# Kernel tuning notes

Hardware: AMD Instinct MI355X
Metric: run time of the kernel (lower is better)

Reference implementation:

```python
import jax, jax.numpy as jnp
import numpy as np

OUTLINER_RATIO = 0.01
RANK = 16
SVD_NITER = 2  # matches torch.svd_lowrank default


def _randomized_svd(A, rank, key, niter=SVD_NITER):
    # torch.svd_lowrank-style randomized range finder + small SVD.
    n, d = A.shape
    Omega = jax.random.normal(key, (d, rank), dtype=A.dtype)
    Q, _ = jnp.linalg.qr(A @ Omega)               # [n, rank]
    for _ in range(niter):
        Q, _ = jnp.linalg.qr(A.T @ Q)             # [d, rank]
        Q, _ = jnp.linalg.qr(A @ Q)               # [n, rank]
    B = Q.T @ A                                   # [rank, d]
    Ub, S, Vh = jnp.linalg.svd(B, full_matrices=False)
    U = Q @ Ub                                    # [n, rank]
    return U, S, Vh


def get_statistics(x, outliner_ratio):
    # threshold such that ~outliner_ratio fraction of |x| exceeds it
    return jnp.quantile(jnp.abs(x), 1.0 - outliner_ratio)


def compress(x, outliner, rank, key):
    # split outliers (kept exactly) from sub-outlier part (low-rank compressed)
    x_outlier = jnp.where(jnp.abs(x) > outliner, x, jnp.zeros((), x.dtype))
    x_sub = (x - x_outlier).reshape(-1, x.shape[-1])   # [N, D]
    U, S, Vh = _randomized_svd(x_sub, rank, key)
    R = Vh.T                                           # [D, rank]
    Rinv = Vh                                          # orthonormal -> pinv = transpose
    L = x_sub @ R                                      # [N, rank]
    return x_outlier, L, R, Rinv


def reference(x, iteration):
    result = jax.nn.silu(x)
    # iteration < 10 branch: compute fresh outlier statistics
    outliner = get_statistics(x, OUTLINER_RATIO)
    # iteration % 50 == 0 -> execute_svd = True (iteration = 0 here)
    key = jax.random.key(42)
    x_outlier_compressed, L, R, Rinv = compress(x, outliner, RANK, key)
    return result, outliner, R, Rinv


def setup_inputs() -> dict:
    key = jax.random.key(0)
    x = jax.random.normal(key, (4, 2048, 4096), dtype=jnp.float32)
    return {"x": x, "iteration": 0}
```

## Files before the change

kernel.cpp:

```cpp
#include <hip/hip_runtime.h>
#include <math.h>


#define N_TOTAL 33554432
#define DDIM    4096
#define NROWS   8192
#define NCHUNK  32
#define RTARGET 33218888u

__device__ __forceinline__ double frcp(double x){
  double r = (double)(1.0f/(float)x);
  r = r*(2.0 - x*r);
  r = r*(2.0 - x*r);
  return r;
}
__device__ __forceinline__ double frsqrt(double x){
  double r = (double)rsqrtf((float)x);
  double hx = 0.5*x;
  r = r*(1.5 - hx*r*r);
  r = r*(1.5 - hx*r*r);
  return r;
}
__device__ __forceinline__ double fsqrt(double x){
  return (x == 0.0) ? 0.0 : x*frsqrt(x);
}

__device__ __forceinline__ double dsign(double a, double b){ return (b >= 0.0) ? fabs(a) : -fabs(a); }

__device__ __forceinline__ void f_slartg(double f, double g, double& c, double& s, double& r){
  if (g == 0.0){ c=1.0; s=0.0; r=f; }
  else if (f == 0.0){ c=0.0; s=dsign(1.0,g); r=fabs(g); }
  else {
    double d2 = f*f+g*g;
    double inv = frsqrt(d2);
    c = fabs(f)*inv;
    r = dsign(d2*inv, f);
    s = g*inv*dsign(1.0,f);
  }
}

__device__ void f_slas2(double f, double g, double h, double& ssmin, double& ssmax){
  double fa=fabs(f), ga=fabs(g), ha=fabs(h);
  double fhmn=fmin(fa,ha), fhmx=fmax(fa,ha);
  if (fhmn == 0.0){
    ssmin=0.0;
    if (fhmx==0.0) ssmax=ga;
    else { double mx=fmax(fhmx,ga), mn=fmin(fhmx,ga); double q=mn*frcp(mx); ssmax = mx*fsqrt(1.0+q*q); }
  } else {
    if (ga < fhmx){
      double rinv = frcp(fhmx);
      double as_=1.0+fhmn*rinv, at=(fhmx-fhmn)*rinv, au=ga*rinv; au=au*au;
      double c=2.0*frcp(fsqrt(as_*as_+au)+fsqrt(at*at+au));
      ssmin=fhmn*c; ssmax=fhmx*frcp(c);
    } else {
      double au=fhmx*frcp(ga);
      if (au==0.0){ ssmin=(fhmn*fhmx)*frcp(ga); ssmax=ga; }
      else {
        double rinv = frcp(fhmx);
        double as_=1.0+fhmn*rinv, at=(fhmx-fhmn)*rinv;
        double c=frcp(fsqrt(1.0+(as_*au)*(as_*au))+fsqrt(1.0+(at*au)*(at*au)));
        ssmin=(fhmn*c)*au; ssmin=ssmin+ssmin; ssmax=ga*frcp(c+c);
      }
    }
  }
}

__device__ void f_slasv2(double f, double g, double h,
                         double& ssmin, double& ssmax, double& snr, double& csr, double& snl, double& csl){
  const double EPSd = 5.9604645e-8;
  double ft=f, fa=fabs(f), ht=h, ha=fabs(h);
  int pmax=1;
  bool swap_=(ha>fa);
  if (swap_){ pmax=3; double t=ft; ft=ht; ht=t; t=fa; fa=ha; ha=t; }
  double gt=g, ga=fabs(g);
  double clt=0, crt=0, slt=0, srt=0;
  if (ga == 0.0){ ssmin=ha; ssmax=fa; clt=1; crt=1; slt=0; srt=0; }
  else {
    bool gasmal=true;
    if (ga > fa){
      pmax=2;
      if ((fa*frcp(ga)) < EPSd){
        gasmal=false;
        ssmax=ga;
        ssmin = (ha>1.0) ? (fa*frcp(ga*frcp(ha))) : ((fa*frcp(ga))*ha);
        clt=1; slt=ht*frcp(gt); srt=1; crt=ft*frcp(gt);
      }
    }
    if (gasmal){
      double d_=fa-ha;
      double fainv = frcp(fa);
      double l_=(d_==fa)?1.0:(d_*fainv);
      double m_=gt*frcp(ft);
      double t_=2.0-l_;
      double mm=m_*m_, tt=t_*t_;
      double s_=fsqrt(tt+mm);
      double r_=(l_==0.0)?fabs(m_):fsqrt(l_*l_+mm);
      double a_=0.5*(s_+r_);
      double ainv = frcp(a_);
      ssmin=ha*ainv;
      ssmax=fa*a_;
      if (mm==0.0){
        t_=(l_==0.0)?(dsign(2.0,ft)*dsign(1.0,gt)):(gt*frcp(dsign(d_,ft))+m_*frcp(t_));
      } else {
        t_=(m_*frcp(s_+t_)+m_*frcp(r_+l_))*(1.0+a_);
      }
      l_=fsqrt(t_*t_+4.0);
      double linv = frcp(l_);
      crt=2.0*linv;
      srt=t_*linv;
      clt=(crt+srt*m_)*ainv;
      slt=(ht*frcp(ft))*srt*ainv;
    }
  }
  if (swap_){ csl=srt; snl=crt; csr=slt; snr=clt; }
  else { csl=clt; snl=slt; csr=crt; snr=srt; }
  double tsign=0.0;
  if (pmax==1) tsign = dsign(1.0,csr)*dsign(1.0,csl)*dsign(1.0,f);
  if (pmax==2) tsign = dsign(1.0,snr)*dsign(1.0,csl)*dsign(1.0,g);
  if (pmax==3) tsign = dsign(1.0,snr)*dsign(1.0,snl)*dsign(1.0,h);
  ssmax = dsign(ssmax, tsign);
  ssmin = dsign(ssmin, tsign*dsign(1.0,f)*dsign(1.0,h));
}

__global__ __launch_bounds__(256) void k_hist1(const float4* __restrict__ x4, unsigned* __restrict__ h1){
  __shared__ unsigned lh[4096];
  for (int i=threadIdx.x; i<4096; i+=256) lh[i]=0u;
  __syncthreads();
  int tid = blockIdx.x*blockDim.x + threadIdx.x;
  int stride = gridDim.x*blockDim.x;
  for (int i = tid; i < N_TOTAL/4; i += stride){
    float4 v = x4[i];
    atomicAdd(&lh[(__float_as_uint(v.x)&0x7FFFFFFFu)>>19], 1u);
    atomicAdd(&lh[(__float_as_uint(v.y)&0x7FFFFFFFu)>>19], 1u);
    atomicAdd(&lh[(__float_as_uint(v.z)&0x7FFFFFFFu)>>19], 1u);
    atomicAdd(&lh[(__float_as_uint(v.w)&0x7FFFFFFFu)>>19], 1u);
  }
  __syncthreads();
  for (int i=threadIdx.x; i<4096; i+=256){ unsigned c=lh[i]; if (c) atomicAdd(&h1[i], c); }
}

__global__ __launch_bounds__(256) void k_siluhist(const float4* __restrict__ x4, float4* __restrict__ o4,
                                                  unsigned* __restrict__ h1){
  __shared__ unsigned lh[4096];
  for (int i=threadIdx.x; i<4096; i+=256) lh[i]=0u;
  __syncthreads();
  int tid = blockIdx.x*blockDim.x + threadIdx.x;
  int stride = gridDim.x*blockDim.x;
  for (int i = tid; i < N_TOTAL/4; i += stride){
    float4 v = x4[i];
    float4 o;
    o.x = v.x / (1.0f + expf(-v.x));
    o.y = v.y / (1.0f + expf(-v.y));
    o.z = v.z / (1.0f + expf(-v.z));
    o.w = v.w / (1.0f + expf(-v.w));
    o4[i] = o;
    atomicAdd(&lh[(__float_as_uint(v.x)&0x7FFFFFFFu)>>19], 1u);
    atomicAdd(&lh[(__float_as_uint(v.y)&0x7FFFFFFFu)>>19], 1u);
    atomicAdd(&lh[(__float_as_uint(v.z)&0x7FFFFFFFu)>>19], 1u);
    atomicAdd(&lh[(__float_as_uint(v.w)&0x7FFFFFFFu)>>19], 1u);
  }
  __syncthreads();
  for (int i=threadIdx.x; i<4096; i+=256){ unsigned c=lh[i]; if (c) atomicAdd(&h1[i], c); }
}

__global__ __launch_bounds__(1024) void k_select1(const unsigned* __restrict__ h1, unsigned* __restrict__ sel){
  __shared__ unsigned ssum[1024];
  int t = threadIdx.x;
  unsigned psum = 0;
  for (int k=0;k<4;++k) psum += h1[t*4+k];
  ssum[t]=psum; __syncthreads();
  for (int off=1; off<1024; off<<=1){
    unsigned v = (t>=off)? ssum[t-off]:0u;
    __syncthreads();
    ssum[t] += v;
    __syncthreads();
  }
  unsigned incl = ssum[t], excl = incl - psum;
  if (excl <= RTARGET && RTARGET < incl){
    unsigned run = excl;
    for (int k=0;k<4;++k){
      unsigned c = h1[t*4+k];
      if (run + c > RTARGET){ sel[1]=(unsigned)(t*4+k); sel[2]=RTARGET-run; break; }
      run += c;
    }
  }
}

__global__ void k_hist2(const float4* __restrict__ x4, unsigned* __restrict__ h2, const unsigned* __restrict__ sel){
  unsigned hstar = sel[1];
  int tid = blockIdx.x*blockDim.x + threadIdx.x;
  int stride = gridDim.x*blockDim.x;
  for (int i = tid; i < N_TOTAL/4; i += stride){
    float4 v = x4[i];
    unsigned b;
    b = __float_as_uint(v.x) & 0x7FFFFFFFu; if ((b>>19)==hstar) atomicAdd(&h2[b&0x7FFFFu],1u);
    b = __float_as_uint(v.y) & 0x7FFFFFFFu; if ((b>>19)==hstar) atomicAdd(&h2[b&0x7FFFFu],1u);
    b = __float_as_uint(v.z) & 0x7FFFFFFFu; if ((b>>19)==hstar) atomicAdd(&h2[b&0x7FFFFu],1u);
    b = __float_as_uint(v.w) & 0x7FFFFFFFu; if ((b>>19)==hstar) atomicAdd(&h2[b&0x7FFFFu],1u);
  }
}

__global__ __launch_bounds__(128) void k_grpsum(const uint4* __restrict__ h2v, unsigned* __restrict__ gs){
  __shared__ unsigned red[128];
  int g = blockIdx.x, t = threadIdx.x;
  uint4 v = h2v[(size_t)g*128 + t];
  red[t] = v.x+v.y+v.z+v.w;
  __syncthreads();
  for (int off=64; off; off>>=1){ if (t<off) red[t] += red[t+off]; __syncthreads(); }
  if (t==0) gs[g] = red[0];
}

__global__ __launch_bounds__(1024) void k_select2b(const unsigned* __restrict__ gs, const unsigned* __restrict__ h2,
                                                   unsigned* __restrict__ sel, float* __restrict__ outScalar){
  __shared__ unsigned ssum[1024];
  __shared__ unsigned sg[2];
  int t = threadIdx.x;
  unsigned target = sel[2], hstar = sel[1];
  unsigned psum = gs[t];
  ssum[t]=psum; __syncthreads();
  for (int off=1; off<1024; off<<=1){
    unsigned v = (t>=off)? ssum[t-off]:0u;
    __syncthreads();
    ssum[t] += v;
    __syncthreads();
  }
  unsigned incl = ssum[t], excl = incl - psum;
  if (excl <= target && target < incl){ sg[0]=(unsigned)t; sg[1]=excl; }
  __syncthreads();
  unsigned g = sg[0], gexcl = sg[1];
  unsigned cnt = (t<512) ? h2[(size_t)g*512 + t] : 0u;
  __syncthreads();
  ssum[t]=cnt; __syncthreads();
  for (int off=1; off<1024; off<<=1){
    unsigned v = (t>=off)? ssum[t-off]:0u;
    __syncthreads();
    ssum[t] += v;
    __syncthreads();
  }
  unsigned incl2 = ssum[t], excl2 = incl2 - cnt;
  unsigned rem = target - gexcl;
  if (t < 512 && excl2 <= rem && rem < incl2){
    unsigned tb = (hstar<<19) | (g*512 + (unsigned)t);
    float tv = __uint_as_float(tb);
    ((float*)sel)[0] = tv;
    *outScalar = tv;
  }
}

__device__ __forceinline__ unsigned rotl32(unsigned x, int r){ return (x<<r)|(x>>(32-r)); }

__device__ __forceinline__ float bits_to_normal(unsigned g){
  float u01 = __uint_as_float((g>>9) | 0x3F800000u) - 1.0f;
  float u = __fadd_rn(__fmul_rn(u01, 2.0f), -0.99999994f);
  u = fmaxf(-0.99999994f, u);
  float xx = __fmul_rn(u,u);
  float w = -log1pf(-xx);
  float p;
  if (w < 5.0f){
    w = __fadd_rn(w, -2.5f);
    p = 2.81022636e-08f;
    p = __fadd_rn(3.43273939e-07f, __fmul_rn(p,w));
    p = __fadd_rn(-3.5233877e-06f, __fmul_rn(p,w));
    p = __fadd_rn(-4.39150654e-06f, __fmul_rn(p,w));
    p = __fadd_rn(0.00021858087f, __fmul_rn(p,w));
    p = __fadd_rn(-0.00125372503f, __fmul_rn(p,w));
    p = __fadd_rn(-0.00417768164f, __fmul_rn(p,w));
    p = __fadd_rn(0.246640727f, __fmul_rn(p,w));
    p = __fadd_rn(1.50140941f, __fmul_rn(p,w));
  } else {
    w = __fadd_rn(sqrtf(w), -3.0f);
    p = -0.000200214257f;
    p = __fadd_rn(0.000100950558f, __fmul_rn(p,w));
    p = __fadd_rn(0.00134934322f, __fmul_rn(p,w));
    p = __fadd_rn(-0.00367342844f, __fmul_rn(p,w));
    p = __fadd_rn(0.00573950773f, __fmul_rn(p,w));
    p = __fadd_rn(-0.0076224613f, __fmul_rn(p,w));
    p = __fadd_rn(0.00943887047f, __fmul_rn(p,w));
    p = __fadd_rn(1.00167406f, __fmul_rn(p,w));
    p = __fadd_rn(2.83297682f, __fmul_rn(p,w));
  }
  return __fmul_rn(__uint_as_float(0x3FB504F3u), __fmul_rn(p,u));
}

#define TF_ROUND(r) { x0 += x1; x1 = rotl32(x1,(r)); x1 ^= x0; }

__global__ void k_omega(float* __restrict__ om){
  unsigned p = blockIdx.x*blockDim.x + threadIdx.x;
  unsigned x0 = p, x1 = 32768u + p;
  const unsigned ks0 = 0u, ks1 = 42u, ks2 = 0x1BD11BDAu ^ 0u ^ 42u;
  x0 += ks0; x1 += ks1;
  TF_ROUND(13) TF_ROUND(15) TF_ROUND(26) TF_ROUND(6)   x0+=ks1; x1+=ks2+1u;
  TF_ROUND(17) TF_ROUND(29) TF_ROUND(16) TF_ROUND(24)  x0+=ks2; x1+=ks0+2u;
  TF_ROUND(13) TF_ROUND(15) TF_ROUND(26) TF_ROUND(6)   x0+=ks0; x1+=ks1+3u;
  TF_ROUND(17) TF_ROUND(29) TF_ROUND(16) TF_ROUND(24)  x0+=ks1; x1+=ks2+4u;
  TF_ROUND(13) TF_ROUND(15) TF_ROUND(26) TF_ROUND(6)   x0+=ks2; x1+=ks0+5u;
  om[p]         = bits_to_normal(x0);
  om[p+32768u]  = bits_to_normal(x1);
}

__global__ __launch_bounds__(256) void k_gemmA(const float* __restrict__ x, const float* __restrict__ W,
                                               float* __restrict__ Y, const float* __restrict__ sel){
  __shared__ double xs[16][128];
  __shared__ double ws[128][16];
  const float t = sel[0];
  const int tid = threadIdx.x;
  const int c = tid & 15, rl = tid >> 4;
  const int row0 = blockIdx.x*16;
  const int c8 = c*8;
  const int wk = (tid*8) >> 4, wc = (tid*8) & 15;
  double acc = 0.0;
  for (int kt = 0; kt < DDIM; kt += 128){
    const float4* p = (const float4*)(x + (size_t)(row0+rl)*DDIM + kt + c8);
    float4 a = p[0], b = p[1];
    xs[rl][c8+0] = (fabsf(a.x) > t) ? 0.0 : (double)a.x;
    xs[rl][c8+1] = (fabsf(a.y) > t) ? 0.0 : (double)a.y;
    xs[rl][c8+2] = (fabsf(a.z) > t) ? 0.0 : (double)a.z;
    xs[rl][c8+3] = (fabsf(a.w) > t) ? 0.0 : (double)a.w;
    xs[rl][c8+4] = (fabsf(b.x) > t) ? 0.0 : (double)b.x;
    xs[rl][c8+5] = (fabsf(b.y) > t) ? 0.0 : (double)b.y;
    xs[rl][c8+6] = (fabsf(b.z) > t) ? 0.0 : (double)b.z;
    xs[rl][c8+7] = (fabsf(b.w) > t) ? 0.0 : (double)b.w;
    const float4* q = (const float4*)(W + (size_t)kt*16 + tid*8);
    float4 wa = q[0], wb = q[1];
    ws[wk][wc+0]=(double)wa.x; ws[wk][wc+1]=(double)wa.y; ws[wk][wc+2]=(double)wa.z; ws[wk][wc+3]=(double)wa.w;
    ws[wk][wc+4]=(double)wb.x; ws[wk][wc+5]=(double)wb.y; ws[wk][wc+6]=(double)wb.z; ws[wk][wc+7]=(double)wb.w;
    __syncthreads();
    #pragma unroll 8
    for (int k=0;k<128;++k) acc += xs[rl][k]*ws[k][c];
    __syncthreads();
  }
  Y[(size_t)(row0+rl)*16 + c] = (float)acc;
}

__global__ __launch_bounds__(256) void k_gemmAT(const float* __restrict__ x, const float* __restrict__ Q,
                                                double* __restrict__ part, const float* __restrict__ sel){
  __shared__ double qs[128][16];
  const float t = sel[0];
  const int tid = threadIdx.x;
  const int d = blockIdx.x*256 + tid;
  const int chunk = blockIdx.y;
  const int i0 = chunk*(NROWS/NCHUNK);
  double acc[16];
  #pragma unroll
  for (int c=0;c<16;++c) acc[c]=0.0;
  for (int it=0; it<NROWS/NCHUNK; it+=128){
    {
      const float4* src = (const float4*)(Q + (size_t)(i0+it)*16) + tid*2;
      float4 a = src[0], b = src[1];
      double* dst = &qs[0][0] + tid*8;
      dst[0]=(double)a.x; dst[1]=(double)a.y; dst[2]=(double)a.z; dst[3]=(double)a.w;
      dst[4]=(double)b.x; dst[5]=(double)b.y; dst[6]=(double)b.z; dst[7]=(double)b.w;
    }
    __syncthreads();
    for (int ii=0; ii<128; ++ii){
      float xv = x[(size_t)(i0+it+ii)*DDIM + d];
      xv = (fabsf(xv) > t) ? 0.0f : xv;
      double xd = (double)xv;
      #pragma unroll
      for (int c=0;c<16;++c) acc[c] += xd*qs[ii][c];
    }
    __syncthreads();
  }
  double* pp = part + ((size_t)chunk*DDIM + d)*16;
  #pragma unroll
  for (int c=0;c<16;++c) pp[c]=acc[c];
}

__global__ void k_reduceT(const double* __restrict__ part, float* __restrict__ outM, int asB, int nchunks){
  int idx = blockIdx.x*blockDim.x + threadIdx.x;
  if (idx >= DDIM*16) return;
  double s = 0.0;
  for (int c=0;c<nchunks;++c) s += part[(size_t)c*DDIM*16 + idx];
  int d = idx >> 4, r = idx & 15;
  if (asB) outM[(size_t)r*DDIM + d] = (float)s;
  else     outM[idx] = (float)s;
}

__global__ __launch_bounds__(256) void k_gramM(const float* __restrict__ M, int rowsPerChunk,
                                               double* __restrict__ part){
  __shared__ float lds[16][17];
  int t = threadIdx.x; int i = t>>4, j = t&15;
  int r0 = blockIdx.x*rowsPerChunk;
  double acc = 0.0;
  for (int rt=0; rt<rowsPerChunk; rt+=16){
    lds[t>>4][t&15] = M[(size_t)(r0+rt+(t>>4))*16 + (t&15)];
    __syncthreads();
    #pragma unroll
    for (int dd=0; dd<16; ++dd) acc += (double)lds[dd][i]*(double)lds[dd][j];
    __syncthreads();
  }
  part[(size_t)blockIdx.x*256 + t] = acc;
}

__global__ __launch_bounds__(256) void k_gramB(const float* __restrict__ B, double* __restrict__ part){
  __shared__ float lds[16][17];
  int t = threadIdx.x; int i = t>>4, j = t&15;
  int d0 = blockIdx.x*256;
  double acc = 0.0;
  for (int dt=0; dt<256; dt+=16){
    lds[t>>4][t&15] = B[(size_t)(t>>4)*DDIM + d0+dt+(t&15)];
    __syncthreads();
    #pragma unroll
    for (int dd=0; dd<16; ++dd) acc += (double)lds[i][dd]*(double)lds[j][dd];
    __syncthreads();
  }
  part[(size_t)blockIdx.x*256 + t] = acc;
}

__global__ __launch_bounds__(256) void k_redchol(const double* __restrict__ part, int nchunks,
                                                 double* __restrict__ Lout, double* __restrict__ Uinv){
  __shared__ double Gs[16][17];
  __shared__ double Vs[16][17];
  int t = threadIdx.x;
  {
    double s = 0.0;
    for (int c=0;c<nchunks;++c) s += part[(size_t)c*256 + t];
    Gs[t>>4][t&15] = s;
  }
  __syncthreads();
  int l = t;
  for (int k=0;k<16;++k){
    if (l==k) Gs[k][k] = fsqrt(Gs[k][k]);
    __syncthreads();
    if (l>k && l<16) Gs[k][l] = Gs[k][l]*frcp(Gs[k][k]);
    __syncthreads();
    if (l>k && l<16){
      double g = Gs[k][l];
      for (int i=k+1;i<=l;++i) Gs[i][l] -= Gs[k][i]*g;
    }
    __syncthreads();
  }
  if (l<16){
    for (int i=0;i<16;++i) Vs[i][l] = 0.0;
    Vs[l][l] = frcp(Gs[l][l]);
    for (int i=l-1;i>=0;--i){
      double s = 0.0;
      for (int k=i+1;k<=l;++k) s += Gs[i][k]*Vs[k][l];
      Vs[i][l] = -s*frcp(Gs[i][i]);
    }
  }
  __syncthreads();
  if (l<16){
    for (int c=0;c<16;++c){
      Lout[l*16+c] = (c<=l) ? Gs[c][l] : 0.0;
      Uinv[l*16+c] = (l<=c) ? Vs[l][c] : 0.0;
    }
  }
}

__global__ __launch_bounds__(256) void k_applyRinv(float* __restrict__ M, const double* __restrict__ Uinv){
  __shared__ double su[256];
  int t = threadIdx.x;
  su[t] = Uinv[t];
  int r = blockIdx.x*16 + (t>>4);
  int j = t & 15;
  const float4* rp = (const float4*)(M + (size_t)r*16);
  float4 v0=rp[0], v1=rp[1], v2=rp[2], v3=rp[3];
  float rowv[16] = {v0.x,v0.y,v0.z,v0.w, v1.x,v1.y,v1.z,v1.w,
                    v2.x,v2.y,v2.z,v2.w, v3.x,v3.y,v3.z,v3.w};
  __syncthreads();
  double acc = 0.0;
  #pragma unroll
  for (int k=0;k<16;++k) acc += (double)rowv[k]*su[k*16+j];
  M[(size_t)r*16 + j] = (float)acc;
}

__global__ __launch_bounds__(64) void k_smallsvd(const double* __restrict__ Lg, double* __restrict__ Wout){
  __shared__ double Lm[16][16];
  __shared__ double VT[16][16];
  __shared__ double A1[16][16];
  __shared__ double dd[16], ee[16], tp[16];
  __shared__ double csv[16], snv[16];
  int l = threadIdx.x;
  for (int idx=l; idx<256; idx+=64){ int r=idx>>4, c=idx&15; Lm[r][c] = (c<=r)? Lg[r*16+c] : 0.0; }
  __syncthreads();
  for (int i=0;i<16;++i){
    double xn2=0.0;
    for (int r=i+1;r<16;++r){ double v=Lm[r][i]; xn2 += v*v; }
    double alpha = Lm[i][i];
    double beta, tauq_, scl;
    if (xn2==0.0){ tauq_=0.0; beta=alpha; scl=0.0; }
    else { beta = -dsign(fsqrt(alpha*alpha+xn2), alpha); tauq_=(beta-alpha)*frcp(beta); scl=frcp(alpha-beta); }
    __syncthreads();
    if (l>i && l<16) Lm[l][i] *= scl;
    __syncthreads();
    dd[i]=beta;
    if (tauq_ != 0.0 && l>i && l<16){
      int j=l;
      double w = Lm[i][j];
      for (int r=i+1;r<16;++r) w += Lm[r][i]*Lm[r][j];
      w *= tauq_;
      Lm[i][j] -= w;
      for (int r=i+1;r<16;++r) Lm[r][j] -= w*Lm[r][i];
    }
    __syncthreads();
    if (i<15){
      double xn2b=0.0;
      for (int c=i+2;c<16;++c){ double v=Lm[i][c]; xn2b+=v*v; }
      double alpha2=Lm[i][i+1];
      double beta2, taup_, scl2;
      if (xn2b==0.0){ taup_=0.0; beta2=alpha2; scl2=0.0; }
      else { beta2=-dsign(fsqrt(alpha2*alpha2+xn2b),alpha2); taup_=(beta2-alpha2)*frcp(beta2); scl2=frcp(alpha2-beta2); }
      __syncthreads();
      if (l>=i+2 && l<16) Lm[i][l] *= scl2;
      __syncthreads();
      ee[i]=beta2; tp[i]=taup_;
      if (taup_!=0.0 && l>i && l<16){
        int r=l;
        double w=Lm[r][i+1];
        for (int c=i+2;c<16;++c) w += Lm[i][c]*Lm[r][c];
        w *= taup_;
        Lm[r][i+1] -= w;
        for (int c=i+2;c<16;++c) Lm[r][c] -= w*Lm[i][c];
      }
      __syncthreads();
    } else { tp[i]=0.0; __syncthreads(); }
  }
  for (int idx=l; idx<256; idx+=64){ int r=idx>>4,c=idx&15; VT[r][c]=(r==c)?1.0:0.0; }
  __syncthreads();
  const double EPSs = 5.9604645e-8;
  const double UNFL = 1.17549435e-38;
  double tol = 10.0*EPSs;
  double sminoa, mu;
  sminoa = mu = fabs(dd[0]);
  if (sminoa != 0.0){
    for (int k=1;k<16;++k){ mu = fabs(dd[k])*(mu*frcp(mu+fabs(ee[k-1]))); sminoa=fmin(sminoa,mu); if (sminoa==0.0) break; }
  }
  sminoa = sminoa/4.0;
  double thresh = fmax(tol*sminoa, 6.0*16.0*16.0*UNFL);
  int m=16, oldll=-1, oldm=-1, idir=0;
  double sminl=0.0;
  int guard=0;
  #define Dv(k) dd[(k)-1]
  #define Ev(k) ee[(k)-1]
  while (m > 1 && guard < 3000){
    ++guard;
    int ll=0; bool split=false;
    double smax_=fabs(Dv(m)), smin_=smax_;
    for (int lll=1; lll<=m-1; ++lll){
      ll = m-lll;
      double abss=fabs(Dv(ll)), abse=fabs(Ev(ll));
      if (abse <= thresh){ split=true; break; }
      smin_=fmin(smin_,abss); smax_=fmax(smax_,fmax(abss,abse));
    }
    if (!split) ll=0;
    else {
      Ev(ll)=0.0;
      if (ll == m-1){ m = m-1; continue; }
    }
    ll = ll+1;
    if (ll == m-1){
      double sigmn,sigmx,sinr,cosr,sinl_,cosl;
      f_slasv2(Dv(m-1), Ev(m-1), Dv(m), sigmn, sigmx, sinr, cosr, sinl_, cosl);
      Dv(m-1)=sigmx; Ev(m-1)=0.0; Dv(m)=sigmn;
      if (l<16){
        double t0 = cosr*VT[m-2][l] + sinr*VT[m-1][l];
        VT[m-1][l] = cosr*VT[m-1][l] - sinr*VT[m-2][l];
        VT[m-2][l] = t0;
      }
      __syncthreads();
      m -= 2; continue;
    }
    if (ll > oldm || m < oldll) idir = (fabs(Dv(ll)) >= fabs(Dv(m))) ? 1 : 2;
    bool cont=false;
    if (idir==1){
      if (fabs(Ev(m-1)) <= tol*fabs(Dv(m))){ Ev(m-1)=0.0; continue; }
      mu = fabs(Dv(ll)); sminl=mu;
      for (int lll=ll; lll<=m-1; ++lll){
        if (fabs(Ev(lll)) <= tol*mu){ Ev(lll)=0.0; cont=true; break; }
        mu = fabs(Dv(lll+1))*(mu*frcp(mu+fabs(Ev(lll)))); sminl=fmin(sminl,mu);
      }
    } else {
      if (fabs(Ev(ll)) <= tol*fabs(Dv(ll))){ Ev(ll)=0.0; continue; }
      mu = fabs(Dv(m)); sminl=mu;
      for (int lll=m-1; lll>=ll; --lll){
        if (fabs(Ev(lll)) <= tol*mu){ Ev(lll)=0.0; cont=true; break; }
        mu = fabs(Dv(lll))*(mu*frcp(mu+fabs(Ev(lll)))); sminl=fmin(sminl,mu);
      }
    }
    if (cont) continue;
    oldll=ll; oldm=m;
    double shift=0.0, rdum;
    if (!( 16.0*tol*(sminl*frcp(smax_)) <= fmax(EPSs, 0.01*tol) )){
      double sll;
      if (idir==1){ sll=fabs(Dv(ll)); f_slas2(Dv(m-1), Ev(m-1), Dv(m), shift, rdum); }
      else        { sll=fabs(Dv(m));  f_slas2(Dv(ll), Ev(ll), Dv(ll+1), shift, rdum); }
      if (sll>0.0){ double q=shift*frcp(sll); if (q*q < EPSs) shift=0.0; }
    }
    if (shift == 0.0){
      if (idir==1){
        double cs=1.0, oldcs=1.0, oldsn=0.0, r_;
        double dcur = Dv(ll);
        for (int i1=ll;i1<=m-1;++i1){
          double cn, snn;
          double a0 = dcur*cs;
          f_slartg(a0, Ev(i1), cn, snn, r_);
          if (i1>ll) Ev(i1-1) = oldsn*r_;
          double dnx = Dv(i1+1);
          double ocn, osn, dnew;
          f_slartg(oldcs*r_, dnx*snn, ocn, osn, dnew);
          Dv(i1)=dnew;
          cs=cn; oldcs=ocn; oldsn=osn;
          csv[i1-1]=cs; snv[i1-1]=snn;
          dcur = dnx;
        }
        double h=dcur*cs;
        Dv(m)=h*oldcs; Ev(m-1)=h*oldsn;
        if (fabs(Ev(m-1))<=thresh) Ev(m-1)=0.0;
        __syncthreads();
        if (l<16){
          double v = VT[ll-1][l];
          for (int i1=ll;i1<=m-1;++i1){
            double c=csv[i1-1], s=snv[i1-1];
            double w = VT[i1][l];
            VT[i1-1][l] = c*v + s*w;
            v = c*w - s*v;
          }
          VT[m-1][l] = v;
        }
      } else {
        double cs=1.0, oldcs=1.0, oldsn=0.0, r_;
        double dcur = Dv(m);
        for (int i1=m;i1>=ll+1;--i1){
          double cn,snn;
          double a0 = dcur*cs;
          f_slartg(a0, Ev(i1-1), cn, snn, r_);
          if (i1<m) Ev(i1)=oldsn*r_;
          double dnx = Dv(i1-1);
          double ocn,osn,dnew;
          f_slartg(oldcs*r_, dnx*snn, ocn, osn, dnew);
          Dv(i1)=dnew;
          cs=cn; oldcs=ocn; oldsn=osn;
          csv[i1-2]=oldcs; snv[i1-2]=-oldsn;
          dcur = dnx;
        }
        double h=dcur*cs;
        Dv(ll)=h*oldcs; Ev(ll)=h*oldsn;
        if (fabs(Ev(ll))<=thresh) Ev(ll)=0.0;
        __syncthreads();
        if (l<16){
          double v = VT[m-1][l];
          for (int i1=m;i1>=ll+1;--i1){
            double c=csv[i1-2], s=snv[i1-2];
            double w = VT[i1-2][l];
            VT[i1-1][l] = c*v - s*w;
            v = c*w + s*v;
          }
          VT[ll-1][l] = v;
        }
      }
    } else {
      if (idir==1){
        double f=(fabs(Dv(ll))-shift)*(dsign(1.0,Dv(ll))+shift*frcp(Dv(ll)));
        double g=Ev(ll);
        double dcur = Dv(ll), ecur = Ev(ll);
        double r_;
        for (int i1=ll;i1<=m-1;++i1){
          double cosr,sinr,cosl,sinl_;
          double dnx = Dv(i1+1);
          f_slartg(f,g,cosr,sinr,r_);
          if (i1>ll) Ev(i1-1)=r_;
          f = cosr*dcur + sinr*ecur;
          double e_mid = cosr*ecur - sinr*dcur;
          g = sinr*dnx;
          double d_mid = cosr*dnx;
          f_slartg(f,g,cosl,sinl_,r_);
          Dv(i1)=r_;
          f = cosl*e_mid + sinl_*d_mid;
          double d_fin = cosl*d_mid - sinl_*e_mid;
          double e_fin = 0.0;
          if (i1 < m-1){ double enx = Ev(i1+1); g = sinl_*enx; e_fin = cosl*enx; }
          csv[i1-1]=cosr; snv[i1-1]=sinr;
          dcur = d_fin; ecur = e_fin;
        }
        Dv(m) = dcur;
        Ev(m-1)=f;
        if (fabs(Ev(m-1))<=thresh) Ev(m-1)=0.0;
        __syncthreads();
        if (l<16){
          double v = VT[ll-1][l];
          for (int i1=ll;i1<=m-1;++i1){
            double c=csv[i1-1], s=snv[i1-1];
            double w = VT[i1][l];
            VT[i1-1][l] = c*v + s*w;
            v = c*w - s*v;
          }
          VT[m-1][l] = v;
        }
      } else {
        double f=(fabs(Dv(m))-shift)*(dsign(1.0,Dv(m))+shift*frcp(Dv(m)));
        double g=Ev(m-1);
        double dcur = Dv(m), ecur = Ev(m-1);
        double r_;
        for (int i1=m;i1>=ll+1;--i1){
          double cosr,sinr,cosl,sinl_;
          double dnx = Dv(i1-1);
          f_slartg(f,g,cosr,sinr,r_);
          if (i1<m) Ev(i1)=r_;
          f = cosr*dcur + sinr*ecur;
          double e_mid = cosr*ecur - sinr*dcur;
          g = sinr*dnx;
          double d_mid = cosr*dnx;
          f_slartg(f,g,cosl,sinl_,r_);
          Dv(i1)=r_;
          f = cosl*e_mid + sinl_*d_mid;
          double d_fin = cosl*d_mid - sinl_*e_mid;
          double e_fin = 0.0;
          if (i1 > ll+1){ double enx = Ev(i1-2); g = sinl_*enx; e_fin = cosl*enx; }
          csv[i1-2]=cosr; snv[i1-2]=-sinr;
          dcur = d_fin; ecur = e_fin;
        }
        Dv(ll) = dcur;
        Ev(ll)=f;
        if (fabs(Ev(ll))<=thresh) Ev(ll)=0.0;
        __syncthreads();
        if (l<16){
          double v = VT[m-1][l];
          for (int i1=m;i1>=ll+1;--i1){
            double c=csv[i1-2], s=snv[i1-2];
            double w = VT[i1-2][l];
            VT[i1-1][l] = c*v - s*w;
            v = c*w + s*v;
          }
          VT[ll-1][l] = v;
        }
      }
    }
    __syncthreads();
  }
  __syncthreads();
  for (int k=1;k<=16;++k){
    if (Dv(k) < 0.0){
      Dv(k) = -Dv(k);
      if (l<16) VT[k-1][l] = -VT[k-1][l];
    }
    __syncthreads();
  }
  for (int i1=1;i1<=15;++i1){
    int isub=1; double smn=Dv(1);
    for (int j=2;j<=17-i1;++j){ if (Dv(j) <= smn){ isub=j; smn=Dv(j);} }
    if (isub != 17-i1){
      double tmpd = Dv(17-i1);
      __syncthreads();
      Dv(isub)=tmpd; Dv(17-i1)=smn;
      if (l<16){ double t2=VT[isub-1][l]; VT[isub-1][l]=VT[16-i1][l]; VT[16-i1][l]=t2; }
    }
    __syncthreads();
  }
  for (int i=14;i>=0;--i){
    double tpv = tp[i];
    if (tpv != 0.0 && l<16){
      int r=l;
      double w = VT[r][i+1];
      for (int c=i+2;c<16;++c) w += VT[r][c]*Lm[i][c];
      w *= tpv;
      VT[r][i+1] -= w;
      for (int c=i+2;c<16;++c) VT[r][c] -= w*Lm[i][c];
    }
    __syncthreads();
  }
  if (l<16){
    int r=l;
    for (int j=15;j>=0;--j){
      double s = VT[r][j];
      for (int k=j+1;k<16;++k) s -= A1[r][k]*Lg[k*16+j];
      A1[r][j] = s*frcp(Lg[j*16+j]);
    }
    for (int j=0;j<16;++j) Wout[r*16+j] = A1[r][j];
  }
  #undef Dv
  #undef Ev
}

__global__ __launch_bounds__(256) void k_formVh2(const float* __restrict__ B, const double* __restrict__ W,
                                                 float* __restrict__ outR, float* __restrict__ outRinv){
  __shared__ double sW[256];
  int t = threadIdx.x;
  sW[t] = W[t];
  __syncthreads();
  int d = blockIdx.x*256 + t;
  double bi[16];
  #pragma unroll
  for (int i=0;i<16;++i) bi[i] = (double)B[(size_t)i*DDIM + d];
  #pragma unroll
  for (int r=0;r<16;++r){
    double s = 0.0;
    #pragma unroll
    for (int i=0;i<16;++i) s += sW[r*16+i]*bi[i];
    float f = (float)s;
    outRinv[(size_t)r*DDIM + d] = f;
    outR[(size_t)d*16 + r] = f;
  }
}

__global__ void k_silu(const float4* __restrict__ x4, float4* __restrict__ o4){
  int tid = blockIdx.x*blockDim.x + threadIdx.x;
  int stride = gridDim.x*blockDim.x;
  for (int i = tid; i < N_TOTAL/4; i += stride){
    float4 v = x4[i];
    float4 o;
    o.x = v.x / (1.0f + expf(-v.x));
    o.y = v.y / (1.0f + expf(-v.y));
    o.z = v.z / (1.0f + expf(-v.z));
    o.w = v.w / (1.0f + expf(-v.w));
    o4[i] = o;
  }
}

static void cholQR(float* M, int N, double* partG, double* Ld, double* Uinvd, hipStream_t stream){
  k_gramM<<<32,256,0,stream>>>(M, N/32, partG);
  k_redchol<<<1,256,0,stream>>>(partG, 32, Ld, Uinvd);
  k_applyRinv<<<N/16,256,0,stream>>>(M, Uinvd);
}

extern "C" void kernel_launch(void* const* d_in, const int* in_sizes, int n_in,
                              void* d_out, int out_size, void* d_ws, size_t ws_size,
                              hipStream_t stream) {
  (void)in_sizes; (void)n_in; (void)out_size;
  const float* x = (const float*)d_in[0];
  float* out = (float*)d_out;
  const size_t NEEDED = 20512768;
  const bool useWs = (d_ws != nullptr) && (ws_size >= NEEDED);
  float* scr = useWs ? (float*)d_ws : out;
  unsigned* h1   = (unsigned*)scr;
  unsigned* h2   = (unsigned*)(scr + 4096);
  unsigned* selu = (unsigned*)(scr + 528384);
  float*    self = (float*)selu;
  unsigned* gs   = (unsigned*)(scr + 528480);
  float* Om = scr + 532480;
  float* Y  = scr + 598016;
  float* T  = scr + 729088;
  float* B  = scr + 794624;
  double* dsm  = (double*)(scr + 860176);
  double* Ld   = dsm;
  double* Uinvd= dsm + 256;
  double* Wd   = dsm + 512;
  double* part = (double*)(scr + 917504);
  double* partG= (double*)(scr + 5111808);
  float* outScalar = out + (size_t)N_TOTAL;
  float* outR      = out + (size_t)N_TOTAL + 1;
  float* outRinv   = out + (size_t)N_TOTAL + 1 + 65536;

  hipMemsetAsync(h1, 0, (4096+524288)*sizeof(unsigned), stream);
  if (useWs){
    k_siluhist<<<2048,256,0,stream>>>((const float4*)x, (float4*)out, h1);
  } else {
    k_hist1<<<1024,256,0,stream>>>((const float4*)x, h1);
  }
  k_select1<<<1,1024,0,stream>>>(h1, selu);
  k_hist2<<<2048,256,0,stream>>>((const float4*)x, h2, selu);
  k_grpsum<<<1024,128,0,stream>>>((const uint4*)h2, gs);
  k_select2b<<<1,1024,0,stream>>>(gs, h2, selu, outScalar);
  k_omega<<<128,256,0,stream>>>(Om);

  k_gemmA<<<512,256,0,stream>>>(x, Om, Y, self);
  cholQR(Y, NROWS, partG, Ld, Uinvd, stream);
  for (int it=0; it<2; ++it){
    k_gemmAT<<<dim3(16,NCHUNK),256,0,stream>>>(x, Y, part, self);
    k_reduceT<<<256,256,0,stream>>>(part, T, 0, NCHUNK);
    cholQR(T, DDIM, partG, Ld, Uinvd, stream);
    k_gemmA<<<512,256,0,stream>>>(x, T, Y, self);
    cholQR(Y, NROWS, partG, Ld, Uinvd, stream);
  }
  k_gemmAT<<<dim3(16,NCHUNK),256,0,stream>>>(x, Y, part, self);
  k_reduceT<<<256,256,0,stream>>>(part, B, 1, NCHUNK);
  k_gramB<<<16,256,0,stream>>>(B, partG);
  k_redchol<<<1,256,0,stream>>>(partG, 16, Ld, Uinvd);
  k_smallsvd<<<1,64,0,stream>>>(Ld, Wd);
  k_formVh2<<<16,256,0,stream>>>(B, Wd, outR, outRinv);
  if (!useWs){
    k_silu<<<2048,256,0,stream>>>((const float4*)x, (float4*)out);
  }
}
```

Measured before the change: 1.261 ms.

## Fuse Gram and Cholesky kernels, vectorize LDS reads, cut Newton steps

Merges each Gram-matrix kernel with the single-block Cholesky reduction, using an atomic last-block counter so the final block performs the reduction, which removes one launch per QR step. It also switches the GEMM inner loops to double2 LDS reads to cut shared-memory instruction count. The small-SVD and Givens helpers now use one Newton refinement step instead of two for reciprocals and rsqrt. That trims latency in the serial single-block SVD but may lose some double-precision accuracy. The workspace layout shifts to make room for the counter, which the memset clears.

```diff
diff --git a/kernel.cpp b/kernel.cpp
--- a/kernel.cpp
+++ b/kernel.cpp
@@ -24,6 +24,19 @@
 __device__ __forceinline__ double fsqrt(double x){
   return (x == 0.0) ? 0.0 : x*frsqrt(x);
 }
+__device__ __forceinline__ double frcp1(double x){
+  double r = (double)(1.0f/(float)x);
+  r = r*(2.0 - x*r);
+  return r;
+}
+__device__ __forceinline__ double frsqrt1(double x){
+  double r = (double)rsqrtf((float)x);
+  r = r*(1.5 - (0.5*x)*r*r);
+  return r;
+}
+__device__ __forceinline__ double fsqrt1(double x){
+  return (x == 0.0) ? 0.0 : x*frsqrt1(x);
+}
 
 __device__ __forceinline__ double dsign(double a, double b){ return (b >= 0.0) ? fabs(a) : -fabs(a); }
 
@@ -32,7 +45,7 @@
   else if (f == 0.0){ c=0.0; s=dsign(1.0,g); r=fabs(g); }
   else {
     double d2 = f*f+g*g;
-    double inv = frsqrt(d2);
+    double inv = frsqrt1(d2);
     c = fabs(f)*inv;
     r = dsign(d2*inv, f);
     s = g*inv*dsign(1.0,f);
@@ -45,21 +58,21 @@
   if (fhmn == 0.0){
     ssmin=0.0;
     if (fhmx==0.0) ssmax=ga;
-    else { double mx=fmax(fhmx,ga), mn=fmin(fhmx,ga); double q=mn*frcp(mx); ssmax = mx*fsqrt(1.0+q*q); }
+    else { double mx=fmax(fhmx,ga), mn=fmin(fhmx,ga); double q=mn*frcp1(mx); ssmax = mx*fsqrt1(1.0+q*q); }
   } else {
     if (ga < fhmx){
-      double rinv = frcp(fhmx);
+      double rinv = frcp1(fhmx);
       double as_=1.0+fhmn*rinv, at=(fhmx-fhmn)*rinv, au=ga*rinv; au=au*au;
-      double c=2.0*frcp(fsqrt(as_*as_+au)+fsqrt(at*at+au));
-      ssmin=fhmn*c; ssmax=fhmx*frcp(c);
+      double c=2.0*frcp1(fsqrt1(as_*as_+au)+fsqrt1(at*at+au));
+      ssmin=fhmn*c; ssmax=fhmx*frcp1(c);
     } else {
-      double au=fhmx*frcp(ga);
-      if (au==0.0){ ssmin=(fhmn*fhmx)*frcp(ga); ssmax=ga; }
+      double au=fhmx*frcp1(ga);
+      if (au==0.0){ ssmin=(fhmn*fhmx)*frcp1(ga); ssmax=ga; }
       else {
-        double rinv = frcp(fhmx);
+        double rinv = frcp1(fhmx);
         double as_=1.0+fhmn*rinv, at=(fhmx-fhmn)*rinv;
-        double c=frcp(fsqrt(1.0+(as_*au)*(as_*au))+fsqrt(1.0+(at*au)*(at*au)));
-        ssmin=(fhmn*c)*au; ssmin=ssmin+ssmin; ssmax=ga*frcp(c+c);
+        double c=frcp1(fsqrt1(1.0+(as_*au)*(as_*au))+fsqrt1(1.0+(at*au)*(at*au)));
+        ssmin=(fhmn*c)*au; ssmin=ssmin+ssmin; ssmax=ga*frcp1(c+c);
       }
     }
   }
@@ -79,37 +92,37 @@
     bool gasmal=true;
     if (ga > fa){
       pmax=2;
-      if ((fa*frcp(ga)) < EPSd){
+      if ((fa*frcp1(ga)) < EPSd){
         gasmal=false;
         ssmax=ga;
-        ssmin = (ha>1.0) ? (fa*frcp(ga*frcp(ha))) : ((fa*frcp(ga))*ha);
-        clt=1; slt=ht*frcp(gt); srt=1; crt=ft*frcp(gt);
+        ssmin = (ha>1.0) ? (fa*frcp1(ga*frcp1(ha))) : ((fa*frcp1(ga))*ha);
+        clt=1; slt=ht*frcp1(gt); srt=1; crt=ft*frcp1(gt);
       }
     }
     if (gasmal){
       double d_=fa-ha;
-      double fainv = frcp(fa);
+      double fainv = frcp1(fa);
       double l_=(d_==fa)?1.0:(d_*fainv);
-      double m_=gt*frcp(ft);
+      double m_=gt*frcp1(ft);
       double t_=2.0-l_;
       double mm=m_*m_, tt=t_*t_;
-      double s_=fsqrt(tt+mm);
-      double r_=(l_==0.0)?fabs(m_):fsqrt(l_*l_+mm);
+      double s_=fsqrt1(tt+mm);
+      double r_=(l_==0.0)?fabs(m_):fsqrt1(l_*l_+mm);
       double a_=0.5*(s_+r_);
-      double ainv = frcp(a_);
+      double ainv = frcp1(a_);
       ssmin=ha*ainv;
       ssmax=fa*a_;
       if (mm==0.0){
-        t_=(l_==0.0)?(dsign(2.0,ft)*dsign(1.0,gt)):(gt*frcp(dsign(d_,ft))+m_*frcp(t_));
+        t_=(l_==0.0)?(dsign(2.0,ft)*dsign(1.0,gt)):(gt*frcp1(dsign(d_,ft))+m_*frcp1(t_));
       } else {
-        t_=(m_*frcp(s_+t_)+m_*frcp(r_+l_))*(1.0+a_);
+        t_=(m_*frcp1(s_+t_)+m_*frcp1(r_+l_))*(1.0+a_);
       }
-      l_=fsqrt(t_*t_+4.0);
-      double linv = frcp(l_);
+      l_=fsqrt1(t_*t_+4.0);
+      double linv = frcp1(l_);
       crt=2.0*linv;
       srt=t_*linv;
       clt=(crt+srt*m_)*ainv;
-      slt=(ht*frcp(ft))*srt*ainv;
+      slt=(ht*frcp1(ft))*srt*ainv;
     }
   }
   if (swap_){ csl=srt; snl=crt; csr=slt; snr=clt; }
@@ -325,8 +338,12 @@
     ws[wk][wc+0]=(double)wa.x; ws[wk][wc+1]=(double)wa.y; ws[wk][wc+2]=(double)wa.z; ws[wk][wc+3]=(double)wa.w;
     ws[wk][wc+4]=(double)wb.x; ws[wk][wc+5]=(double)wb.y; ws[wk][wc+6]=(double)wb.z; ws[wk][wc+7]=(double)wb.w;
     __syncthreads();
-    #pragma unroll 8
-    for (int k=0;k<128;++k) acc += xs[rl][k]*ws[k][c];
+    #pragma unroll
+    for (int k=0;k<128;k+=2){
+      double2 xv2 = *(const double2*)&xs[rl][k];
+      acc += xv2.x*ws[k][c];
+      acc += xv2.y*ws[k+1][c];
+    }
     __syncthreads();
   }
   Y[(size_t)(row0+rl)*16 + c] = (float)acc;
@@ -357,7 +374,11 @@
       xv = (fabsf(xv) > t) ? 0.0f : xv;
       double xd = (double)xv;
       #pragma unroll
-      for (int c=0;c<16;++c) acc[c] += xd*qs[ii][c];
+      for (int c2=0;c2<8;++c2){
+        double2 q2 = *(const double2*)&qs[ii][c2*2];
+        acc[c2*2]   += xd*q2.x;
+        acc[c2*2+1] += xd*q2.y;
+      }
     }
     __syncthreads();
   }
@@ -376,42 +397,8 @@
   else     outM[idx] = (float)s;
 }
 
-__global__ __launch_bounds__(256) void k_gramM(const float* __restrict__ M, int rowsPerChunk,
-                                               double* __restrict__ part){
-  __shared__ float lds[16][17];
-  int t = threadIdx.x; int i = t>>4, j = t&15;
-  int r0 = blockIdx.x*rowsPerChunk;
-  double acc = 0.0;
-  for (int rt=0; rt<rowsPerChunk; rt+=16){
-    lds[t>>4][t&15] = M[(size_t)(r0+rt+(t>>4))*16 + (t&15)];
-    __syncthreads();
-    #pragma unroll
-    for (int dd=0; dd<16; ++dd) acc += (double)lds[dd][i]*(double)lds[dd][j];
-    __syncthreads();
-  }
-  part[(size_t)blockIdx.x*256 + t] = acc;
-}
-
-__global__ __launch_bounds__(256) void k_gramB(const float* __restrict__ B, double* __restrict__ part){
-  __shared__ float lds[16][17];
-  int t = threadIdx.x; int i = t>>4, j = t&15;
-  int d0 = blockIdx.x*256;
-  double acc = 0.0;
-  for (int dt=0; dt<256; dt+=16){
-    lds[t>>4][t&15] = B[(size_t)(t>>4)*DDIM + d0+dt+(t&15)];
-    __syncthreads();
-    #pragma unroll
-    for (int dd=0; dd<16; ++dd) acc += (double)lds[i][dd]*(double)lds[j][dd];
-    __syncthreads();
-  }
-  part[(size_t)blockIdx.x*256 + t] = acc;
-}
-
-__global__ __launch_bounds__(256) void k_redchol(const double* __restrict__ part, int nchunks,
-                                                 double* __restrict__ Lout, double* __restrict__ Uinv){
-  __shared__ double Gs[16][17];
-  __shared__ double Vs[16][17];
-  int t = threadIdx.x;
+__device__ void redchol_body(const double* part, int nchunks, double* Lout, double* Uinv,
+                             double (*Gs)[17], double (*Vs)[17], int t){
   {
     double s = 0.0;
     for (int c=0;c<nchunks;++c) s += part[(size_t)c*256 + t];
@@ -446,6 +433,64 @@
       Uinv[l*16+c] = (l<=c) ? Vs[l][c] : 0.0;
     }
   }
+}
+
+__global__ __launch_bounds__(256) void k_gramMC(const float* __restrict__ M, int rowsPerChunk,
+                                                double* __restrict__ part,
+                                                double* __restrict__ Lout, double* __restrict__ Uinv,
+                                                unsigned* __restrict__ ctr){
+  __shared__ float lds[16][17];
+  __shared__ double Gs[16][17];
+  __shared__ double Vs[16][17];
+  __shared__ unsigned slast;
+  int t = threadIdx.x; int i = t>>4, j = t&15;
+  int r0 = blockIdx.x*rowsPerChunk;
+  double acc = 0.0;
+  for (int rt=0; rt<rowsPerChunk; rt+=16){
+    lds[t>>4][t&15] = M[(size_t)(r0+rt+(t>>4))*16 + (t&15)];
+    __syncthreads();
+    #pragma unroll
+    for (int dd2=0; dd2<16; ++dd2) acc += (double)lds[dd2][i]*(double)lds[dd2][j];
+    __syncthreads();
+  }
+  part[(size_t)blockIdx.x*256 + t] = acc;
+  __threadfence();
+  if (t==0) slast = atomicAdd(ctr, 1u);
+  __syncthreads();
+  if (slast != gridDim.x-1u) return;
+  __threadfence();
+  redchol_body(part, (int)gridDim.x, Lout, Uinv, Gs, Vs, t);
+  __syncthreads();
+  if (t==0) *ctr = 0u;
+}
+
+__global__ __launch_bounds__(256) void k_gramBC(const float* __restrict__ B,
+                                                double* __restrict__ part,
+                                                double* __restrict__ Lout, double* __restrict__ Uinv,
+                                                unsigned* __restrict__ ctr){
+  __shared__ float lds[16][17];
+  __shared__ double Gs[16][17];
+  __shared__ double Vs[16][17];
+  __shared__ unsigned slast;
+  int t = threadIdx.x; int i = t>>4, j = t&15;
+  int d0 = blockIdx.x*256;
+  double acc = 0.0;
+  for (int dt=0; dt<256; dt+=16){
+    lds[t>>4][t&15] = B[(size_t)(t>>4)*DDIM + d0+dt+(t&15)];
+    __syncthreads();
+    #pragma unroll
+    for (int dd2=0; dd2<16; ++dd2) acc += (double)lds[i][dd2]*(double)lds[j][dd2];
+    __syncthreads();
+  }
+  part[(size_t)blockIdx.x*256 + t] = acc;
+  __threadfence();
+  if (t==0) slast = atomicAdd(ctr, 1u);
+  __syncthreads();
+  if (slast != gridDim.x-1u) return;
+  __threadfence();
+  redchol_body(part, (int)gridDim.x, Lout, Uinv, Gs, Vs, t);
+  __syncthreads();
+  if (t==0) *ctr = 0u;
 }
 
 __global__ __launch_bounds__(256) void k_applyRinv(float* __restrict__ M, const double* __restrict__ Uinv){
@@ -480,7 +525,7 @@
     double alpha = Lm[i][i];
     double beta, tauq_, scl;
     if (xn2==0.0){ tauq_=0.0; beta=alpha; scl=0.0; }
-    else { beta = -dsign(fsqrt(alpha*alpha+xn2), alpha); tauq_=(beta-alpha)*frcp(beta); scl=frcp(alpha-beta); }
+    else { beta = -dsign(fsqrt1(alpha*alpha+xn2), alpha); tauq_=(beta-alpha)*frcp1(beta); scl=frcp1(alpha-beta); }
     __syncthreads();
     if (l>i && l<16) Lm[l][i] *= scl;
     __syncthreads();
@@ -500,7 +545,7 @@
       double alpha2=Lm[i][i+1];
       double beta2, taup_, scl2;
       if (xn2b==0.0){ taup_=0.0; beta2=alpha2; scl2=0.0; }
-      else { beta2=-dsign(fsqrt(alpha2*alpha2+xn2b),alpha2); taup_=(beta2-alpha2)*frcp(beta2); scl2=frcp(alpha2-beta2); }
+      else { beta2=-dsign(fsqrt1(alpha2*alpha2+xn2b),alpha2); taup_=(beta2-alpha2)*frcp1(beta2); scl2=frcp1(alpha2-beta2); }
       __syncthreads();
       if (l>=i+2 && l<16) Lm[i][l] *= scl2;
       __syncthreads();
@@ -524,7 +569,7 @@
   double sminoa, mu;
   sminoa = mu = fabs(dd[0]);
   if (sminoa != 0.0){
-    for (int k=1;k<16;++k){ mu = fabs(dd[k])*(mu*frcp(mu+fabs(ee[k-1]))); sminoa=fmin(sminoa,mu); if (sminoa==0.0) break; }
+    for (int k=1;k<16;++k){ mu = fabs(dd[k])*(mu*frcp1(mu+fabs(ee[k-1]))); sminoa=fmin(sminoa,mu); if (sminoa==0.0) break; }
   }
   sminoa = sminoa/4.0;
   double thresh = fmax(tol*sminoa, 6.0*16.0*16.0*UNFL);
@@ -568,24 +613,24 @@
       mu = fabs(Dv(ll)); sminl=mu;
       for (int lll=ll; lll<=m-1; ++lll){
         if (fabs(Ev(lll)) <= tol*mu){ Ev(lll)=0.0; cont=true; break; }
-        mu = fabs(Dv(lll+1))*(mu*frcp(mu+fabs(Ev(lll)))); sminl=fmin(sminl,mu);
+        mu = fabs(Dv(lll+1))*(mu*frcp1(mu+fabs(Ev(lll)))); sminl=fmin(sminl,mu);
       }
     } else {
       if (fabs(Ev(ll)) <= tol*fabs(Dv(ll))){ Ev(ll)=0.0; continue; }
       mu = fabs(Dv(m)); sminl=mu;
       for (int lll=m-1; lll>=ll; --lll){
         if (fabs(Ev(lll)) <= tol*mu){ Ev(lll)=0.0; cont=true; break; }
-        mu = fabs(Dv(lll))*(mu*frcp(mu+fabs(Ev(lll)))); sminl=fmin(sminl,mu);
+        mu = fabs(Dv(lll))*(mu*frcp1(mu+fabs(Ev(lll)))); sminl=fmin(sminl,mu);
       }
     }
     if (cont) continue;
     oldll=ll; oldm=m;
     double shift=0.0, rdum;
-    if (!( 16.0*tol*(sminl*frcp(smax_)) <= fmax(EPSs, 0.01*tol) )){
+    if (!( 16.0*tol*(sminl*frcp1(smax_)) <= fmax(EPSs, 0.01*tol) )){
       double sll;
       if (idir==1){ sll=fabs(Dv(ll)); f_slas2(Dv(m-1), Ev(m-1), Dv(m), shift, rdum); }
       else        { sll=fabs(Dv(m));  f_slas2(Dv(ll), Ev(ll), Dv(ll+1), shift, rdum); }
-      if (sll>0.0){ double q=shift*frcp(sll); if (q*q < EPSs) shift=0.0; }
+      if (sll>0.0){ double q=shift*frcp1(sll); if (q*q < EPSs) shift=0.0; }
     }
     if (shift == 0.0){
       if (idir==1){
@@ -651,7 +696,7 @@
       }
     } else {
       if (idir==1){
-        double f=(fabs(Dv(ll))-shift)*(dsign(1.0,Dv(ll))+shift*frcp(Dv(ll)));
+        double f=(fabs(Dv(ll))-shift)*(dsign(1.0,Dv(ll))+shift*frcp1(Dv(ll)));
         double g=Ev(ll);
         double dcur = Dv(ll), ecur = Ev(ll);
         double r_;
@@ -688,7 +733,7 @@
           VT[m-1][l] = v;
         }
       } else {
-        double f=(fabs(Dv(m))-shift)*(dsign(1.0,Dv(m))+shift*frcp(Dv(m)));
+        double f=(fabs(Dv(m))-shift)*(dsign(1.0,Dv(m))+shift*frcp1(Dv(m)));
         double g=Ev(m-1);
         double dcur = Dv(m), ecur = Ev(m-1);
         double r_;
@@ -764,7 +809,7 @@
     for (int j=15;j>=0;--j){
       double s = VT[r][j];
       for (int k=j+1;k<16;++k) s -= A1[r][k]*Lg[k*16+j];
-      A1[r][j] = s*frcp(Lg[j*16+j]);
+      A1[r][j] = s*frcp1(Lg[j*16+j]);
     }
     for (int j=0;j<16;++j) Wout[r*16+j] = A1[r][j];
   }
@@ -807,9 +852,9 @@
   }
 }
 
-static void cholQR(float* M, int N, double* partG, double* Ld, double* Uinvd, hipStream_t stream){
-  k_gramM<<<32,256,0,stream>>>(M, N/32, partG);
-  k_redchol<<<1,256,0,stream>>>(partG, 32, Ld, Uinvd);
+static void cholQR(float* M, int N, double* partG, double* Ld, double* Uinvd, unsigned* ctr,
+                   hipStream_t stream){
+  k_gramMC<<<32,256,0,stream>>>(M, N/32, partG, Ld, Uinvd, ctr);
   k_applyRinv<<<N/16,256,0,stream>>>(M, Uinvd);
 }
 
@@ -819,29 +864,30 @@
   (void)in_sizes; (void)n_in; (void)out_size;
   const float* x = (const float*)d_in[0];
   float* out = (float*)d_out;
-  const size_t NEEDED = 20512768;
+  const size_t NEEDED = 20512832;
   const bool useWs = (d_ws != nullptr) && (ws_size >= NEEDED);
   float* scr = useWs ? (float*)d_ws : out;
   unsigned* h1   = (unsigned*)scr;
   unsigned* h2   = (unsigned*)(scr + 4096);
-  unsigned* selu = (unsigned*)(scr + 528384);
+  unsigned* ctr  = (unsigned*)(scr + 528384);
+  unsigned* selu = (unsigned*)(scr + 528400);
   float*    self = (float*)selu;
-  unsigned* gs   = (unsigned*)(scr + 528480);
-  float* Om = scr + 532480;
-  float* Y  = scr + 598016;
-  float* T  = scr + 729088;
-  float* B  = scr + 794624;
-  double* dsm  = (double*)(scr + 860176);
+  unsigned* gs   = (unsigned*)(scr + 528496);
+  float* Om = scr + 532496;
+  float* Y  = scr + 598032;
+  float* T  = scr + 729104;
+  float* B  = scr + 794640;
+  double* dsm  = (double*)(scr + 860192);
   double* Ld   = dsm;
   double* Uinvd= dsm + 256;
   double* Wd   = dsm + 512;
-  double* part = (double*)(scr + 917504);
-  double* partG= (double*)(scr + 5111808);
+  double* part = (double*)(scr + 917520);
+  double* partG= (double*)(scr + 5111824);
   float* outScalar = out + (size_t)N_TOTAL;
   float* outR      = out + (size_t)N_TOTAL + 1;
   float* outRinv   = out + (size_t)N_TOTAL + 1 + 65536;
 
-  hipMemsetAsync(h1, 0, (4096+524288)*sizeof(unsigned), stream);
+  hipMemsetAsync(h1, 0, (4096+524288+16)*sizeof(unsigned), stream);
   if (useWs){
     k_siluhist<<<2048,256,0,stream>>>((const float4*)x, (float4*)out, h1);
   } else {
@@ -854,18 +900,17 @@
   k_omega<<<128,256,0,stream>>>(Om);
 
   k_gemmA<<<512,256,0,stream>>>(x, Om, Y, self);
-  cholQR(Y, NROWS, partG, Ld, Uinvd, stream);
+  cholQR(Y, NROWS, partG, Ld, Uinvd, ctr, stream);
   for (int it=0; it<2; ++it){
     k_gemmAT<<<dim3(16,NCHUNK),256,0,stream>>>(x, Y, part, self);
     k_reduceT<<<256,256,0,stream>>>(part, T, 0, NCHUNK);
-    cholQR(T, DDIM, partG, Ld, Uinvd, stream);
+    cholQR(T, DDIM, partG, Ld, Uinvd, ctr, stream);
     k_gemmA<<<512,256,0,stream>>>(x, T, Y, self);
-    cholQR(Y, NROWS, partG, Ld, Uinvd, stream);
+    cholQR(Y, NROWS, partG, Ld, Uinvd, ctr, stream);
   }
   k_gemmAT<<<dim3(16,NCHUNK),256,0,stream>>>(x, Y, part, self);
   k_reduceT<<<256,256,0,stream>>>(part, B, 1, NCHUNK);
-  k_gramB<<<16,256,0,stream>>>(B, partG);
-  k_redchol<<<1,256,0,stream>>>(partG, 16, Ld, Uinvd);
+  k_gramBC<<<16,256,0,stream>>>(B, partG, Ld, Uinvd, ctr);
   k_smallsvd<<<1,64,0,stream>>>(Ld, Wd);
   k_formVh2<<<16,256,0,stream>>>(B, Wd, outR, outRinv);
   if (!useWs){
```

Result: no change. 1.265 ms (+0.3%).
